# Kernel optimization log

Hardware: AMD Instinct MI355X
Metric: run time of the kernel (lower is better)

Reference implementation:

```python
import jax, jax.numpy as jnp
import numpy as np

B, S, H = 4, 4096, 256

def setup_inputs() -> dict:
    key = jax.random.key(0)
    ks = jax.random.split(key, 7)
    s = 1.0 / np.sqrt(H)
    return {
        "x": jax.random.normal(ks[0], (B, S, H), dtype=jnp.float32),
        "Wq": jax.random.normal(ks[1], (H, H), dtype=jnp.float32) * s,
        "bq": jax.random.normal(ks[2], (H,), dtype=jnp.float32) * 0.01,
        "Wk": jax.random.normal(ks[3], (H, H), dtype=jnp.float32) * s,
        "bk": jax.random.normal(ks[4], (H,), dtype=jnp.float32) * 0.01,
        "Wv": jax.random.normal(ks[5], (H, H), dtype=jnp.float32) * s,
        "bv": jax.random.normal(ks[6], (H,), dtype=jnp.float32) * 0.01,
    }

def reference(x, Wq, bq, Wk, bk, Wv, bv):
    # Linear projections (torch Linear: x @ W^T + b; here W stored as [in,out])
    Q = jnp.einsum('bsh,hd->bsd', x, Wq) + bq
    K = jnp.einsum('bsh,hd->bsd', x, Wk) + bk
    V = jnp.einsum('bsh,hd->bsd', x, Wv) + bv
    scale = 1.0 / jnp.sqrt(jnp.float32(x.shape[-1]))
    scores = jnp.einsum('bqd,bkd->bqk', Q, K) * scale  # [B,S,S]
    weights = jax.nn.softmax(scores, axis=-1)
    return jnp.einsum('bqk,bkd->bqd', weights, V)
```

## Files before the change

kernel.cpp:

```cpp
#include <hip/hip_runtime.h>
#include <hip/hip_bf16.h>
#include <stdint.h>
#include <stddef.h>


typedef __bf16 bf16;
typedef _Float16 f16;
typedef __attribute__((ext_vector_type(4))) __bf16 bf16x4;
typedef __attribute__((ext_vector_type(8))) __bf16 bf16x8;
typedef __attribute__((ext_vector_type(4))) float f32x4;
typedef __attribute__((ext_vector_type(4))) _Float16 f16x4;
typedef __attribute__((ext_vector_type(8))) _Float16 f16x8;

#define S_LEN 4096
#define HDIM  256
#define PSTRIDE ((size_t)16384 * 256)

__device__ __forceinline__ f32x4 mfma16(bf16x8 a, bf16x8 b, f32x4 c) {
  return __builtin_amdgcn_mfma_f32_16x16x32_bf16(a, b, c, 0, 0, 0);
}

__device__ __forceinline__ void gld_lds16(const void* g, void* l) {
  __builtin_amdgcn_global_load_lds(
      (const __attribute__((address_space(1))) void*)g,
      (__attribute__((address_space(3))) void*)l, 16, 0, 0);
}

__device__ __forceinline__ float fast_exp2(float x) {
  float r;
  asm("v_exp_f32 %0, %1" : "=v"(r) : "v"(x));
  return r;
}

__global__ __launch_bounds__(256) void wt_kernel(
    const float* __restrict__ Wq, const float* __restrict__ Wk,
    const float* __restrict__ Wv, bf16* __restrict__ WT) {
  __shared__ float tile[32][33];
  int bid = blockIdx.x;
  int m = bid >> 6;
  int t = bid & 63;
  int hb = (t >> 3) * 32;
  int db = (t & 7) * 32;
  const float* W = (m == 0) ? Wq : (m == 1) ? Wk : Wv;
  bf16* o = WT + m * 65536;
  int ty = threadIdx.x >> 3;
  int tx = threadIdx.x & 7;
  float4 v = *(const float4*)(W + (size_t)(hb + ty) * 256 + db + tx * 4);
  tile[ty][tx * 4 + 0] = v.x; tile[ty][tx * 4 + 1] = v.y;
  tile[ty][tx * 4 + 2] = v.z; tile[ty][tx * 4 + 3] = v.w;
  __syncthreads();
  bf16x4 h = {(bf16)tile[tx * 4 + 0][ty], (bf16)tile[tx * 4 + 1][ty],
              (bf16)tile[tx * 4 + 2][ty], (bf16)tile[tx * 4 + 3][ty]};
  *(bf16x4*)(o + (size_t)(db + ty) * 256 + hb + tx * 4) = h;
}

__global__ __launch_bounds__(256, 3) void proj_kernel(
    const float* __restrict__ x, const bf16* __restrict__ WT,
    const float* __restrict__ bq, const float* __restrict__ bk,
    const float* __restrict__ bv,
    bf16* __restrict__ Qb, char* __restrict__ KV) {
  __shared__ __align__(16) char smem[34816];
  int tid = threadIdx.x;
  int row0 = blockIdx.x * 64;
  int m = blockIdx.y;

#pragma unroll
  for (int i = 0; i < 16; ++i) {
    int c = i * 256 + tid;
    int r = c >> 6, c4 = c & 63;
    float4 v = *(const float4*)(x + (size_t)(row0 + r) * 256 + c4 * 4);
    bf16x4 b4 = {(bf16)v.x, (bf16)v.y, (bf16)v.z, (bf16)v.w};
    *(bf16x4*)(smem + r * 512 + ((c4 * 8) ^ ((r & 7) << 4))) = b4;
  }
  __syncthreads();

  int w = tid >> 6, lane = tid & 63, lg = lane >> 4, l15 = lane & 15;
  int ar = w * 16 + l15;
  int swz = (l15 & 7) << 4;
  bf16x8 af[8];
#pragma unroll
  for (int ks = 0; ks < 8; ++ks)
    af[ks] = *(const bf16x8*)(smem + ar * 512 + ((ks * 64 + lg * 16) ^ swz));
  __syncthreads();

  int b = row0 >> 12, t0 = (row0 & 4095) >> 5;
  const bf16* Wm = WT + m * 65536;
  const float* bias = (m == 0) ? bq : (m == 1) ? bk : bv;

#pragma unroll
  for (int i = 0; i < 4; ++i) {
    int c = w * 4 + i;
    gld_lds16(Wm + (c * 16 + l15) * 256 + lg * 8, smem + c * 1024 + lane * 16);
  }
  __syncthreads();

  f32x4 acc[16];
#pragma unroll
  for (int dt = 0; dt < 16; ++dt) acc[dt] = f32x4{0.f, 0.f, 0.f, 0.f};

  for (int ks = 0; ks < 8; ++ks) {
    const char* wb = smem + (ks & 1) * 16384;
    if (ks + 1 < 8) {
      char* wn = smem + ((ks + 1) & 1) * 16384;
#pragma unroll
      for (int i = 0; i < 4; ++i) {
        int c = w * 4 + i;
        gld_lds16(Wm + (c * 16 + l15) * 256 + (ks + 1) * 32 + lg * 8,
                  wn + c * 1024 + lane * 16);
      }
    }
    __builtin_amdgcn_s_setprio(1);
#pragma unroll
    for (int dt = 0; dt < 16; ++dt) {
      bf16x8 wf = *(const bf16x8*)(wb + dt * 1024 + lane * 16);
      acc[dt] = mfma16(af[ks], wf, acc[dt]);
    }
    __builtin_amdgcn_s_setprio(0);
    __syncthreads();
  }

  if (m == 0) {
#pragma unroll
    for (int dt = 0; dt < 16; ++dt) {
      float bb = bias[dt * 16 + l15];
#pragma unroll
      for (int rr = 0; rr < 4; ++rr) {
        int srow = row0 + w * 16 + 4 * lg + rr;
        Qb[(size_t)srow * 256 + dt * 16 + l15] = (bf16)(acc[dt][rr] + bb);
      }
    }
  } else if (m == 1) {
    bf16* sm16 = (bf16*)smem;
#pragma unroll
    for (int dt = 0; dt < 16; ++dt) {
      float bb = bias[dt * 16 + l15];
#pragma unroll
      for (int rr = 0; rr < 4; ++rr) {
        int sl = w * 16 + 4 * lg + rr;
        sm16[sl * 264 + dt * 16 + l15] = (bf16)(acc[dt][rr] + bb);
      }
    }
    __syncthreads();
    int tt = tid >> 7, c = (tid >> 3) & 15, j0 = (tid & 7) * 8;
    char* dst = KV + ((size_t)(b * 128 + t0 + tt)) * 32768 + c * 1024 + j0 * 16;
#pragma unroll
    for (int u = 0; u < 8; ++u) {
      int l = j0 + u;
      bf16x8 v8 = *(const bf16x8*)(sm16 + (tt * 32 + (c & 1) * 16 + (l & 15)) * 264
                                   + (c >> 1) * 32 + (l >> 4) * 8);
      *(bf16x8*)(dst + u * 16) = v8;
    }
  } else {
    bf16* smV = (bf16*)smem;
#pragma unroll
    for (int dt = 0; dt < 16; ++dt) {
      float bb = bias[dt * 16 + l15];
      bf16x4 h = {(bf16)(acc[dt][0] + bb), (bf16)(acc[dt][1] + bb),
                  (bf16)(acc[dt][2] + bb), (bf16)(acc[dt][3] + bb)};
      *(bf16x4*)(smV + (dt * 16 + l15) * 68 + w * 16 + 4 * lg) = h;
    }
    __syncthreads();
    int tt = tid >> 7, c = (tid >> 3) & 15, j0 = (tid & 7) * 8;
    char* dst = KV + ((size_t)(b * 128 + t0 + tt)) * 32768 + 16384
                + c * 1024 + j0 * 16;
#pragma unroll
    for (int u = 0; u < 8; ++u) {
      int l = j0 + u;
      const bf16* p = smV + (c * 16 + (l & 15)) * 68 + tt * 32 + 4 * (l >> 4);
      bf16x4 lo = *(const bf16x4*)p;
      bf16x4 hi = *(const bf16x4*)(p + 16);
      bf16x8 v8 = __builtin_shufflevector(lo, hi, 0, 1, 2, 3, 4, 5, 6, 7);
      *(bf16x8*)(dst + u * 16) = v8;
    }
  }
}

__global__ __launch_bounds__(256, 2) void attn_kernel(
    const bf16* __restrict__ Qb, const char* __restrict__ KV,
    f16* __restrict__ P, float* __restrict__ ml, int nsplit, int ntiles) {
  __shared__ __align__(16) char smem[65536];

  int id = blockIdx.x;
  int b, sp, qb;
  if (nsplit == 4)      { int g = id & 15; b = g & 3;  sp = g >> 2; qb = id >> 4; }
  else if (nsplit == 2) { int g = id & 7;  b = g >> 1; sp = g & 1;  qb = id >> 3; }
  else                  { b = id & 3; sp = 0; qb = id >> 2; }

  int tid = threadIdx.x;
  int w = tid >> 6, lane = tid & 63, lg = lane >> 4, l15 = lane & 15;

  const char* kvsrc = KV + ((size_t)(b * 128 + sp * ntiles)) * 32768;

  int qrow0 = b * S_LEN + qb * 128 + w * 32 + l15;
  bf16x8 qf[2][8];
#pragma unroll
  for (int qs = 0; qs < 2; ++qs) {
    const bf16* Qr = Qb + (size_t)(qrow0 + qs * 16) * HDIM;
#pragma unroll
    for (int ks = 0; ks < 8; ++ks)
      qf[qs][ks] = *(const bf16x8*)(Qr + ks * 32 + lg * 8);
  }

  f32x4 acc[2][16];
#pragma unroll
  for (int qs = 0; qs < 2; ++qs)
#pragma unroll
    for (int dt = 0; dt < 16; ++dt) acc[qs][dt] = f32x4{0.f, 0.f, 0.f, 0.f};
  float lsum[2] = {0.f, 0.f};
  const float C = 0.09016844005556021f;

#pragma unroll
  for (int i = 0; i < 8; ++i)
    gld_lds16(kvsrc + i * 4096 + tid * 16, smem + i * 4096 + tid * 16);
  __syncthreads();

  for (int t = 0; t < ntiles; ++t) {
    int cur = (t & 1) << 15;
    const char* s2 = kvsrc + (size_t)(t + 1) * 32768;
    char* d2 = smem + (cur ^ 32768);
    if (t + 1 < ntiles) {
#pragma unroll
      for (int i = 0; i < 4; ++i)
        gld_lds16(s2 + i * 4096 + tid * 16, d2 + i * 4096 + tid * 16);
    }
    const char* kb = smem + cur;
    const char* vb = kb + 16384;

    f32x4 st[2][2];
    st[0][0] = f32x4{0.f, 0.f, 0.f, 0.f}; st[0][1] = st[0][0];
    st[1][0] = st[0][0];                   st[1][1] = st[0][0];
    __builtin_amdgcn_s_setprio(1);
#pragma unroll
    for (int ks = 0; ks < 8; ++ks) {
      bf16x8 k0 = *(const bf16x8*)(kb + (ks * 2 + 0) * 1024 + lane * 16);
      bf16x8 k1 = *(const bf16x8*)(kb + (ks * 2 + 1) * 1024 + lane * 16);
      st[0][0] = mfma16(k0, qf[0][ks], st[0][0]);
      st[1][0] = mfma16(k0, qf[1][ks], st[1][0]);
      st[0][1] = mfma16(k1, qf[0][ks], st[0][1]);
      st[1][1] = mfma16(k1, qf[1][ks], st[1][1]);
    }
    __builtin_amdgcn_s_setprio(0);

    if (t + 1 < ntiles) {
#pragma unroll
      for (int i = 4; i < 8; ++i)
        gld_lds16(s2 + i * 4096 + tid * 16, d2 + i * 4096 + tid * 16);
    }

    bf16x8 pf[2];
#pragma unroll
    for (int qs = 0; qs < 2; ++qs) {
      float ps = 0.f;
#pragma unroll
      for (int e = 0; e < 8; ++e) {
        float pv = fast_exp2(st[qs][e >> 2][e & 3] * C);
        ps += pv;
        pf[qs][e] = (bf16)pv;
      }
      lsum[qs] += ps;
    }

    __builtin_amdgcn_s_setprio(1);
#pragma unroll
    for (int dt = 0; dt < 16; ++dt) {
      bf16x8 vf = *(const bf16x8*)(vb + dt * 1024 + lane * 16);
      acc[0][dt] = mfma16(vf, pf[0], acc[0][dt]);
      acc[1][dt] = mfma16(vf, pf[1], acc[1][dt]);
    }
    __builtin_amdgcn_s_setprio(0);
    __syncthreads();
  }

  f16* Pp = P + (size_t)sp * PSTRIDE;
#pragma unroll
  for (int qs = 0; qs < 2; ++qs) {
    float l = lsum[qs];
    l += __shfl_xor(l, 16, 64);
    l += __shfl_xor(l, 32, 64);
    int qrow = qrow0 + qs * 16;
    f16* prow = Pp + (size_t)qrow * HDIM;
#pragma unroll
    for (int dt = 0; dt < 16; ++dt) {
      f32x4 a = acc[qs][dt];
      f16x4 h = {(f16)a[0], (f16)a[1], (f16)a[2], (f16)a[3]};
      *(f16x4*)(prow + dt * 16 + 4 * lg) = h;
    }
    if (lane < 16) ml[sp * 16384 + qrow] = l;
  }
}

__global__ __launch_bounds__(256) void combine_kernel(
    float* __restrict__ out, const f16* __restrict__ P,
    const float* __restrict__ ml, int nsplit) {
  int chunk = blockIdx.x * 256 + threadIdx.x;
  int q = chunk >> 5;
  size_t base = (size_t)chunk * 8;

  float l = 0.f;
  float o[8] = {0.f, 0.f, 0.f, 0.f, 0.f, 0.f, 0.f, 0.f};
  for (int sp = 0; sp < nsplit; ++sp) {
    l += ml[sp * 16384 + q];
    f16x8 v = *(const f16x8*)(P + sp * PSTRIDE + base);
#pragma unroll
    for (int j = 0; j < 8; ++j) o[j] += (float)v[j];
  }
  float inv = 1.0f / l;
  f32x4 o0 = {o[0] * inv, o[1] * inv, o[2] * inv, o[3] * inv};
  f32x4 o1 = {o[4] * inv, o[5] * inv, o[6] * inv, o[7] * inv};
  *(f32x4*)(out + base) = o0;
  *(f32x4*)(out + base + 4) = o1;
}

extern "C" void kernel_launch(void* const* d_in, const int* in_sizes, int n_in,
                              void* d_out, int out_size, void* d_ws, size_t ws_size,
                              hipStream_t stream) {
  (void)in_sizes; (void)n_in; (void)out_size;
  const float* x  = (const float*)d_in[0];
  const float* Wq = (const float*)d_in[1];
  const float* bq = (const float*)d_in[2];
  const float* Wk = (const float*)d_in[3];
  const float* bk = (const float*)d_in[4];
  const float* Wv = (const float*)d_in[5];
  const float* bv = (const float*)d_in[6];

  char* ws = (char*)d_ws;
  bf16*  Qb = (bf16*)(ws);
  char*  KV = ws + (8u << 20);
  bf16*  WT = (bf16*)(ws + (24u << 20));
  float* ml = (float*)(ws + (24u << 20) + (512u << 10));
  f16*   P  = (f16*)(ws + (26u << 20));

  size_t need4 = ((size_t)26 << 20) + 4 * ((size_t)8 << 20);
  size_t need2 = ((size_t)26 << 20) + 2 * ((size_t)8 << 20);
  int nsplit = (ws_size >= need4) ? 4 : (ws_size >= need2) ? 2 : 1;
  int ntiles = (S_LEN / nsplit) / 32;
  int nblocks = 128 * nsplit;

  wt_kernel<<<192, 256, 0, stream>>>(Wq, Wk, Wv, WT);
  proj_kernel<<<dim3(256, 3), 256, 0, stream>>>(x, WT, bq, bk, bv, Qb, KV);
  attn_kernel<<<nblocks, 256, 0, stream>>>(Qb, KV, P, ml, nsplit, ntiles);
  combine_kernel<<<2048, 256, 0, stream>>>((float*)d_out, P, ml, nsplit);
}
```

Before: 108.1 us.

## Fuse split-KV combine into attention kernel and relax prefetch barriers

Removes the separate combine kernel. An atomic counter per (batch, query block) now marks which attention block finishes last, and that block reduces the partial outputs and writes the final normalized result. Inside the tile loop, the full __syncthreads is replaced with explicit vmcnt waits plus s_barrier, so the second half of the next tile's LDS prefetch can stay in flight across the barriers. This saves one kernel launch and its tail, at the cost of a memset, atomics and fences, and a serialized combine in the last-finishing block.

```diff
diff --git a/kernel.cpp b/kernel.cpp
--- a/kernel.cpp
+++ b/kernel.cpp
@@ -31,6 +31,17 @@
   asm("v_exp_f32 %0, %1" : "=v"(r) : "v"(x));
   return r;
 }
+
+#define BAR_VMCNT4() do { \
+  asm volatile("s_waitcnt vmcnt(4)" ::: "memory"); \
+  __builtin_amdgcn_s_barrier(); \
+  asm volatile("" ::: "memory"); \
+  __builtin_amdgcn_sched_barrier(0); } while (0)
+#define BAR_VMCNT0() do { \
+  asm volatile("s_waitcnt vmcnt(0)" ::: "memory"); \
+  __builtin_amdgcn_s_barrier(); \
+  asm volatile("" ::: "memory"); \
+  __builtin_amdgcn_sched_barrier(0); } while (0)
 
 __global__ __launch_bounds__(256) void wt_kernel(
     const float* __restrict__ Wq, const float* __restrict__ Wk,
@@ -177,7 +188,8 @@
 
 __global__ __launch_bounds__(256, 2) void attn_kernel(
     const bf16* __restrict__ Qb, const char* __restrict__ KV,
-    f16* __restrict__ P, float* __restrict__ ml, int nsplit, int ntiles) {
+    f16* __restrict__ P, float* __restrict__ ml, float* __restrict__ out,
+    int* __restrict__ cnt, int nsplit, int ntiles) {
   __shared__ __align__(16) char smem[65536];
 
   int id = blockIdx.x;
@@ -212,19 +224,21 @@
 #pragma unroll
   for (int i = 0; i < 8; ++i)
     gld_lds16(kvsrc + i * 4096 + tid * 16, smem + i * 4096 + tid * 16);
-  __syncthreads();
+  BAR_VMCNT0();
 
   for (int t = 0; t < ntiles; ++t) {
     int cur = (t & 1) << 15;
+    const char* kb = smem + cur;
+    const char* vb = kb + 16384;
     const char* s2 = kvsrc + (size_t)(t + 1) * 32768;
     char* d2 = smem + (cur ^ 32768);
-    if (t + 1 < ntiles) {
+    bool pre = (t + 1 < ntiles);
+
+    if (pre) {
 #pragma unroll
       for (int i = 0; i < 4; ++i)
         gld_lds16(s2 + i * 4096 + tid * 16, d2 + i * 4096 + tid * 16);
     }
-    const char* kb = smem + cur;
-    const char* vb = kb + 16384;
 
     f32x4 st[2][2];
     st[0][0] = f32x4{0.f, 0.f, 0.f, 0.f}; st[0][1] = st[0][0];
@@ -241,7 +255,9 @@
     }
     __builtin_amdgcn_s_setprio(0);
 
-    if (t + 1 < ntiles) {
+    if (pre) BAR_VMCNT4(); else BAR_VMCNT0();
+
+    if (pre) {
 #pragma unroll
       for (int i = 4; i < 8; ++i)
         gld_lds16(s2 + i * 4096 + tid * 16, d2 + i * 4096 + tid * 16);
@@ -268,7 +284,8 @@
       acc[1][dt] = mfma16(vf, pf[1], acc[1][dt]);
     }
     __builtin_amdgcn_s_setprio(0);
-    __syncthreads();
+
+    if (pre) BAR_VMCNT4();
   }
 
   f16* Pp = P + (size_t)sp * PSTRIDE;
@@ -287,28 +304,37 @@
     }
     if (lane < 16) ml[sp * 16384 + qrow] = l;
   }
-}
-
-__global__ __launch_bounds__(256) void combine_kernel(
-    float* __restrict__ out, const f16* __restrict__ P,
-    const float* __restrict__ ml, int nsplit) {
-  int chunk = blockIdx.x * 256 + threadIdx.x;
-  int q = chunk >> 5;
-  size_t base = (size_t)chunk * 8;
-
-  float l = 0.f;
-  float o[8] = {0.f, 0.f, 0.f, 0.f, 0.f, 0.f, 0.f, 0.f};
-  for (int sp = 0; sp < nsplit; ++sp) {
-    l += ml[sp * 16384 + q];
-    f16x8 v = *(const f16x8*)(P + sp * PSTRIDE + base);
-#pragma unroll
-    for (int j = 0; j < 8; ++j) o[j] += (float)v[j];
-  }
-  float inv = 1.0f / l;
-  f32x4 o0 = {o[0] * inv, o[1] * inv, o[2] * inv, o[3] * inv};
-  f32x4 o1 = {o[4] * inv, o[5] * inv, o[6] * inv, o[7] * inv};
-  *(f32x4*)(out + base) = o0;
-  *(f32x4*)(out + base + 4) = o1;
+
+  __syncthreads();
+  int* flag = (int*)smem;
+  if (tid == 0) {
+    __threadfence();
+    int old = atomicAdd(&cnt[b * 32 + qb], 1);
+    *flag = (old == nsplit - 1) ? 1 : 0;
+  }
+  __syncthreads();
+  if (*flag) {
+    __threadfence();
+    size_t base = ((size_t)(b * 4096 + qb * 128)) * 256;
+    for (int k = 0; k < 16; ++k) {
+      int ci = k * 256 + tid;
+      int qrow = b * 4096 + qb * 128 + (ci >> 5);
+      size_t off = base + (size_t)ci * 8;
+      float l = 0.f;
+      float o[8] = {0.f, 0.f, 0.f, 0.f, 0.f, 0.f, 0.f, 0.f};
+      for (int sp2 = 0; sp2 < nsplit; ++sp2) {
+        l += ml[sp2 * 16384 + qrow];
+        f16x8 v = *(const f16x8*)(P + sp2 * PSTRIDE + off);
+#pragma unroll
+        for (int j = 0; j < 8; ++j) o[j] += (float)v[j];
+      }
+      float inv = 1.0f / l;
+      f32x4 o0 = {o[0] * inv, o[1] * inv, o[2] * inv, o[3] * inv};
+      f32x4 o1 = {o[4] * inv, o[5] * inv, o[6] * inv, o[7] * inv};
+      *(f32x4*)(out + off) = o0;
+      *(f32x4*)(out + off + 4) = o1;
+    }
+  }
 }
 
 extern "C" void kernel_launch(void* const* d_in, const int* in_sizes, int n_in,
@@ -324,11 +350,12 @@
   const float* bv = (const float*)d_in[6];
 
   char* ws = (char*)d_ws;
-  bf16*  Qb = (bf16*)(ws);
-  char*  KV = ws + (8u << 20);
-  bf16*  WT = (bf16*)(ws + (24u << 20));
-  float* ml = (float*)(ws + (24u << 20) + (512u << 10));
-  f16*   P  = (f16*)(ws + (26u << 20));
+  bf16*  Qb  = (bf16*)(ws);
+  char*  KV  = ws + (8u << 20);
+  bf16*  WT  = (bf16*)(ws + (24u << 20));
+  float* ml  = (float*)(ws + (24u << 20) + (512u << 10));
+  int*   cnt = (int*)(ws + (25u << 20));
+  f16*   P   = (f16*)(ws + (26u << 20));
 
   size_t need4 = ((size_t)26 << 20) + 4 * ((size_t)8 << 20);
   size_t need2 = ((size_t)26 << 20) + 2 * ((size_t)8 << 20);
@@ -336,8 +363,9 @@
   int ntiles = (S_LEN / nsplit) / 32;
   int nblocks = 128 * nsplit;
 
+  hipMemsetAsync(cnt, 0, 512, stream);
   wt_kernel<<<192, 256, 0, stream>>>(Wq, Wk, Wv, WT);
   proj_kernel<<<dim3(256, 3), 256, 0, stream>>>(x, WT, bq, bk, bv, Qb, KV);
-  attn_kernel<<<nblocks, 256, 0, stream>>>(Qb, KV, P, ml, nsplit, ntiles);
-  combine_kernel<<<2048, 256, 0, stream>>>((float*)d_out, P, ml, nsplit);
-}
+  attn_kernel<<<nblocks, 256, 0, stream>>>(Qb, KV, P, ml, (float*)d_out,
+                                           cnt, nsplit, ntiles);
+}
```

After: 163.6 us. +51.2%, slower.
